# Kernel tuning notes

Measured on AMD Instinct MI355X. Metric: run time of the kernel, lower is better.

## Reference

```python
import jax, jax.numpy as jnp
import numpy as np

S, H, A = 8192, 4096, 1024

def setup_inputs() -> dict:
    key = jax.random.key(0)
    ks = jax.random.split(key, 8)
    return {
        "encoder_outputs": jax.random.normal(ks[0], (S, H), jnp.float32),
        "hidden": jax.random.normal(ks[1], (H,), jnp.float32),
        "U_w": jax.random.normal(ks[2], (A, H), jnp.float32) * (1.0 / np.sqrt(H)),
        "U_b": jax.random.normal(ks[3], (A,), jnp.float32) * 0.01,
        "W_w": jax.random.normal(ks[4], (A, H), jnp.float32) * (1.0 / np.sqrt(H)),
        "W_b": jax.random.normal(ks[5], (A,), jnp.float32) * 0.01,
        "V_w": jax.random.normal(ks[6], (1, A), jnp.float32) * (1.0 / np.sqrt(A)),
        "V_b": jax.random.normal(ks[7], (1,), jnp.float32) * 0.01,
    }

def reference(encoder_outputs, hidden, U_w, U_b, W_w, W_b, V_w, V_b):
    # Bahdanau additive attention ('add' mode).
    W_hidden = hidden @ W_w.T + W_b                      # [A]
    U_encode = encoder_outputs @ U_w.T + U_b             # [S, A]
    poly_tanh = jnp.tanh(U_encode + W_hidden)            # [S, A]
    scores = poly_tanh @ V_w.T + V_b                     # [S, 1]
    attn = jax.nn.softmax(scores, axis=0)                # softmax over sequence
    context = attn.T @ encoder_outputs                   # [1, H]
    return context[None]                                 # [1, 1, H] (matches torch bmm)
```

## Files before the change

kernel.cpp:

```cpp
#include <hip/hip_runtime.h>

typedef __attribute__((ext_vector_type(8))) short short8;
typedef __attribute__((ext_vector_type(4))) float f32x4;

#define S_DIM 8192
#define H_DIM 4096
#define A_DIM 1024

__device__ __forceinline__ short f2bf(float x) {
  unsigned u = __float_as_uint(x);
  u += 0x7fffu + ((u >> 16) & 1u);
  return (short)(u >> 16);
}

__device__ __forceinline__ float bf2f(short b) {
  return __uint_as_float(((unsigned)(unsigned short)b) << 16);
}

__device__ __forceinline__ void gload16(const void* g, void* l) {
  __builtin_amdgcn_global_load_lds(
      (const __attribute__((address_space(1))) void*)g,
      (__attribute__((address_space(3))) void*)l, 16, 0, 0);
}

__global__ __launch_bounds__(256) void comb_kernel(const float* __restrict__ hidden,
                                                   const float* __restrict__ Ww,
                                                   const float* __restrict__ Wb,
                                                   const float* __restrict__ Ub,
                                                   float* __restrict__ comb) {
  const int wave = threadIdx.x >> 6;
  const int lane = threadIdx.x & 63;
  const int a = blockIdx.x * 4 + wave;
  const float* row = Ww + (size_t)a * H_DIM;
  float acc = 0.f;
  for (int k = lane * 4; k < H_DIM; k += 64 * 4) {
    float4 w = *(const float4*)(row + k);
    float4 h = *(const float4*)(hidden + k);
    acc += w.x * h.x + w.y * h.y + w.z * h.z + w.w * h.w;
  }
  #pragma unroll
  for (int mk = 1; mk < 64; mk <<= 1) acc += __shfl_xor(acc, mk);
  if (lane == 0) comb[a] = acc + Wb[a] + Ub[a];
}

__global__ __launch_bounds__(256) void cvt_kernel(const float* __restrict__ src,
                                                  unsigned short* __restrict__ dst,
                                                  int n8) {
  const int stride = gridDim.x * blockDim.x;
  for (int i = blockIdx.x * blockDim.x + threadIdx.x; i < n8; i += stride) {
    float4 a = ((const float4*)src)[(size_t)i * 2];
    float4 b = ((const float4*)src)[(size_t)i * 2 + 1];
    short8 o;
    o[0] = f2bf(a.x); o[1] = f2bf(a.y); o[2] = f2bf(a.z); o[3] = f2bf(a.w);
    o[4] = f2bf(b.x); o[5] = f2bf(b.y); o[6] = f2bf(b.z); o[7] = f2bf(b.w);
    ((short8*)dst)[i] = o;
  }
}

__global__ __launch_bounds__(512, 2) void gemm_score_8p_kernel(
    const unsigned short* __restrict__ A,
    const unsigned short* __restrict__ B,
    const float* __restrict__ comb,
    const float* __restrict__ Vw,
    float* __restrict__ scores) {
  __shared__ __align__(16) unsigned short sA[3][256 * 64];
  __shared__ __align__(16) unsigned short sB[3][128 * 64];

  const int tid  = threadIdx.x;
  const int lane = tid & 63;
  const int wave = tid >> 6;
  const int wm = wave >> 1;
  const int wn = wave & 1;
  const int m0 = blockIdx.x * 256;
  const int n0 = blockIdx.y * 128;

  const int permEl = (((lane & 7) ^ (lane >> 3)) * 8);
  const unsigned short* gA = A + (size_t)(m0 + wave * 32 + (lane >> 3)) * H_DIM + permEl;
  const unsigned short* gB = B + (size_t)(n0 + wave * 16 + (lane >> 3)) * H_DIM + permEl;

  #define STAGE(kt, bf) do {                                                  \
    const unsigned short* pa_ = gA + (size_t)(kt) * 64;                       \
    const unsigned short* pb_ = gB + (size_t)(kt) * 64;                       \
    _Pragma("unroll")                                                         \
    for (int l_ = 0; l_ < 4; ++l_)                                            \
      gload16(pa_ + (size_t)l_ * 8 * H_DIM, &sA[bf][(wave * 4 + l_) * 512]);  \
    _Pragma("unroll")                                                         \
    for (int l_ = 0; l_ < 2; ++l_)                                            \
      gload16(pb_ + (size_t)l_ * 8 * H_DIM, &sB[bf][(wave * 2 + l_) * 512]);  \
  } while (0)

  const int rA  = lane & 15;
  const int grp = lane >> 4;
  const int lx  = lane & 7;

  f32x4 acc[4][4];
  const f32x4 zero = {0.f, 0.f, 0.f, 0.f};
  #pragma unroll
  for (int i = 0; i < 4; ++i)
    #pragma unroll
    for (int j = 0; j < 4; ++j) acc[i][j] = zero;

  STAGE(0, 0);
  STAGE(1, 1);
  asm volatile("s_waitcnt vmcnt(6)");
  __builtin_amdgcn_s_barrier();
  __builtin_amdgcn_sched_barrier(0);

  const int NT = H_DIM / 64;
  for (int t = 0; t < NT; ++t) {
    const int cur = t % 3;
    if (t + 2 < NT) STAGE(t + 2, (t + 2) % 3);

    const unsigned short* a_ = sA[cur];
    const unsigned short* b_ = sB[cur];
    #pragma unroll
    for (int ks = 0; ks < 2; ++ks) {
      short8 af[4], bfr[4];
      #pragma unroll
      for (int i = 0; i < 4; ++i)
        af[i] = *(const short8*)&a_[(wm * 64 + i * 16 + rA) * 64 + (((ks * 4 + grp) ^ lx) * 8)];
      #pragma unroll
      for (int j = 0; j < 4; ++j)
        bfr[j] = *(const short8*)&b_[(wn * 64 + j * 16 + rA) * 64 + (((ks * 4 + grp) ^ lx) * 8)];
      __builtin_amdgcn_s_setprio(1);
      #pragma unroll
      for (int i = 0; i < 4; ++i)
        #pragma unroll
        for (int j = 0; j < 4; ++j)
          acc[i][j] = __builtin_amdgcn_mfma_f32_16x16x32_bf16(af[i], bfr[j], acc[i][j], 0, 0, 0);
      __builtin_amdgcn_s_setprio(0);
    }

    __builtin_amdgcn_sched_barrier(0);
    if (t < NT - 2) asm volatile("s_waitcnt vmcnt(6)");
    else            asm volatile("s_waitcnt vmcnt(0)");
    __builtin_amdgcn_s_barrier();
    __builtin_amdgcn_sched_barrier(0);
  }
  #undef STAGE

  float vwv[4], cbv[4];
  #pragma unroll
  for (int j = 0; j < 4; ++j) {
    const int col = n0 + wn * 64 + j * 16 + rA;
    vwv[j] = Vw[col];
    cbv[j] = comb[col];
  }
  #pragma unroll
  for (int i = 0; i < 4; ++i) {
    #pragma unroll
    for (int r = 0; r < 4; ++r) {
      float s = 0.f;
      #pragma unroll
      for (int j = 0; j < 4; ++j)
        s += vwv[j] * tanhf(acc[i][j][r] + cbv[j]);
      s += __shfl_xor(s, 1);
      s += __shfl_xor(s, 2);
      s += __shfl_xor(s, 4);
      s += __shfl_xor(s, 8);
      if (rA == 0) {
        const int grow = m0 + wm * 64 + i * 16 + grp * 4 + r;
        atomicAdd(&scores[grow], s);
      }
    }
  }
}

__global__ __launch_bounds__(1024) void softmax_kernel(const float* __restrict__ scores,
                                                       float* __restrict__ attn) {
  __shared__ float redm[16];
  __shared__ float reds[16];
  const int tid = threadIdx.x;
  const int lane = tid & 63, wid = tid >> 6;
  float v[8];
  float m = -3.0e38f;
  #pragma unroll
  for (int i = 0; i < 8; ++i) { v[i] = scores[i * 1024 + tid]; m = fmaxf(m, v[i]); }
  #pragma unroll
  for (int mk = 1; mk < 64; mk <<= 1) m = fmaxf(m, __shfl_xor(m, mk));
  if (lane == 0) redm[wid] = m;
  __syncthreads();
  float M = redm[0];
  #pragma unroll
  for (int j = 1; j < 16; ++j) M = fmaxf(M, redm[j]);
  float e[8]; float s = 0.f;
  #pragma unroll
  for (int i = 0; i < 8; ++i) { e[i] = __expf(v[i] - M); s += e[i]; }
  #pragma unroll
  for (int mk = 1; mk < 64; mk <<= 1) s += __shfl_xor(s, mk);
  if (lane == 0) reds[wid] = s;
  __syncthreads();
  float T = 0.f;
  #pragma unroll
  for (int j = 0; j < 16; ++j) T += reds[j];
  const float inv = 1.f / T;
  #pragma unroll
  for (int i = 0; i < 8; ++i) attn[i * 1024 + tid] = e[i] * inv;
}

__global__ __launch_bounds__(256) void context_bf_kernel(const unsigned short* __restrict__ Ebf,
                                                         const float* __restrict__ attn,
                                                         float* __restrict__ partial) {
  const int h0 = (blockIdx.x * 256 + threadIdx.x) * 8;
  const int s0 = blockIdx.y * 64;
  float acc[8] = {0.f, 0.f, 0.f, 0.f, 0.f, 0.f, 0.f, 0.f};
  for (int s = s0; s < s0 + 64; ++s) {
    const float w = attn[s];
    short8 e = *(const short8*)(Ebf + (size_t)s * H_DIM + h0);
    #pragma unroll
    for (int j = 0; j < 8; ++j) acc[j] += w * bf2f(e[j]);
  }
  float* p = partial + (size_t)blockIdx.y * H_DIM + h0;
  #pragma unroll
  for (int j = 0; j < 8; ++j) p[j] = acc[j];
}

__global__ __launch_bounds__(256) void context_reduce_kernel(const float* __restrict__ partial,
                                                             float* __restrict__ out) {
  const int h = blockIdx.x * 256 + threadIdx.x;
  float acc = 0.f;
  #pragma unroll 8
  for (int y = 0; y < 128; ++y) acc += partial[(size_t)y * H_DIM + h];
  out[h] = acc;
}


#define LDSW 40
__global__ __launch_bounds__(256) void gemm_score_kernel(const float* __restrict__ E,
                                                         const float* __restrict__ Uw,
                                                         const float* __restrict__ comb,
                                                         const float* __restrict__ Vw,
                                                         float* __restrict__ scores) {
  __shared__ __align__(16) short sA[128 * LDSW];
  __shared__ __align__(16) short sB[128 * LDSW];
  const int tid  = threadIdx.x;
  const int lane = tid & 63;
  const int wave = tid >> 6;
  const int wm = wave >> 1, wn = wave & 1;
  const int m0 = blockIdx.x * 128;
  const int n0 = blockIdx.y * 128;
  const int sr = tid >> 1;
  const int sh = tid & 1;
  const float* gA = E  + (size_t)(m0 + sr) * H_DIM + sh * 16;
  const float* gB = Uw + (size_t)(n0 + sr) * H_DIM + sh * 16;
  alignas(16) float fa[16], fb[16];
  #pragma unroll
  for (int j = 0; j < 4; ++j) {
    *(float4*)&fa[j * 4] = *(const float4*)(gA + j * 4);
    *(float4*)&fb[j * 4] = *(const float4*)(gB + j * 4);
  }
  f32x4 acc[4][4];
  const f32x4 zero = {0.f, 0.f, 0.f, 0.f};
  #pragma unroll
  for (int i = 0; i < 4; ++i)
    #pragma unroll
    for (int j = 0; j < 4; ++j) acc[i][j] = zero;
  short* wA = &sA[sr * LDSW + sh * 16];
  short* wB = &sB[sr * LDSW + sh * 16];
  const int NK = H_DIM / 32;
  for (int kt = 0; kt < NK; ++kt) {
    short8 ca0, ca1, cb0, cb1;
    #pragma unroll
    for (int j = 0; j < 8; ++j) {
      ca0[j] = f2bf(fa[j]);     ca1[j] = f2bf(fa[8 + j]);
      cb0[j] = f2bf(fb[j]);     cb1[j] = f2bf(fb[8 + j]);
    }
    __syncthreads();
    *(short8*)(wA)     = ca0;
    *(short8*)(wA + 8) = ca1;
    *(short8*)(wB)     = cb0;
    *(short8*)(wB + 8) = cb1;
    __syncthreads();
    if (kt + 1 < NK) {
      const float* pA = gA + (kt + 1) * 32;
      const float* pB = gB + (kt + 1) * 32;
      #pragma unroll
      for (int j = 0; j < 4; ++j) {
        *(float4*)&fa[j * 4] = *(const float4*)(pA + j * 4);
        *(float4*)&fb[j * 4] = *(const float4*)(pB + j * 4);
      }
    }
    short8 af[4], bfr[4];
    #pragma unroll
    for (int i = 0; i < 4; ++i)
      af[i] = *(const short8*)&sA[(wm * 64 + i * 16 + (lane & 15)) * LDSW + (lane >> 4) * 8];
    #pragma unroll
    for (int j = 0; j < 4; ++j)
      bfr[j] = *(const short8*)&sB[(wn * 64 + j * 16 + (lane & 15)) * LDSW + (lane >> 4) * 8];
    #pragma unroll
    for (int i = 0; i < 4; ++i)
      #pragma unroll
      for (int j = 0; j < 4; ++j)
        acc[i][j] = __builtin_amdgcn_mfma_f32_16x16x32_bf16(af[i], bfr[j], acc[i][j], 0, 0, 0);
  }
  float vwv[4], cbv[4];
  #pragma unroll
  for (int j = 0; j < 4; ++j) {
    const int col = n0 + wn * 64 + j * 16 + (lane & 15);
    vwv[j] = Vw[col];
    cbv[j] = comb[col];
  }
  #pragma unroll
  for (int i = 0; i < 4; ++i) {
    #pragma unroll
    for (int r = 0; r < 4; ++r) {
      float s = 0.f;
      #pragma unroll
      for (int j = 0; j < 4; ++j)
        s += vwv[j] * tanhf(acc[i][j][r] + cbv[j]);
      s += __shfl_xor(s, 1);
      s += __shfl_xor(s, 2);
      s += __shfl_xor(s, 4);
      s += __shfl_xor(s, 8);
      if ((lane & 15) == 0) {
        const int grow = m0 + wm * 64 + i * 16 + (lane >> 4) * 4 + r;
        atomicAdd(&scores[grow], s);
      }
    }
  }
}

__global__ __launch_bounds__(256) void context_kernel(const float* __restrict__ E,
                                                      const float* __restrict__ attn,
                                                      float* __restrict__ out) {
  const int h  = blockIdx.x * 256 + threadIdx.x;
  const int s0 = blockIdx.y * 256;
  float acc = 0.f;
  #pragma unroll 4
  for (int s = s0; s < s0 + 256; ++s)
    acc += attn[s] * E[(size_t)s * H_DIM + h];
  atomicAdd(&out[h], acc);
}


extern "C" void kernel_launch(void* const* d_in, const int* in_sizes, int n_in,
                              void* d_out, int out_size, void* d_ws, size_t ws_size,
                              hipStream_t stream) {
  const float* E   = (const float*)d_in[0];
  const float* hid = (const float*)d_in[1];
  const float* Uw  = (const float*)d_in[2];
  const float* Ub  = (const float*)d_in[3];
  const float* Ww  = (const float*)d_in[4];
  const float* Wb  = (const float*)d_in[5];
  const float* Vw  = (const float*)d_in[6];

  float* out    = (float*)d_out;
  float* ws     = (float*)d_ws;
  float* comb   = ws;
  float* scores = ws + 1024;
  float* attn   = ws + 1024 + 8192;
  float* ctxp   = ws + 17408;
  const size_t CTXP = (size_t)128 * H_DIM;

  unsigned short* Ebf  = (unsigned short*)(ws + 17408 + CTXP);
  unsigned short* Uwbf = Ebf + (size_t)S_DIM * H_DIM;
  const size_t NEED = ((size_t)17408 + CTXP) * 4
                    + ((size_t)S_DIM + A_DIM) * H_DIM * 2;

  hipMemsetAsync(scores, 0, S_DIM * sizeof(float), stream);

  comb_kernel<<<A_DIM / 4, 256, 0, stream>>>(hid, Ww, Wb, Ub, comb);

  if (ws_size >= NEED) {
    cvt_kernel<<<2048, 256, 0, stream>>>(E, Ebf, (int)((size_t)S_DIM * H_DIM / 8));
    cvt_kernel<<<512, 256, 0, stream>>>(Uw, Uwbf, (int)((size_t)A_DIM * H_DIM / 8));

    gemm_score_8p_kernel<<<dim3(S_DIM / 256, A_DIM / 128), 512, 0, stream>>>(
        Ebf, Uwbf, comb, Vw, scores);

    softmax_kernel<<<1, 1024, 0, stream>>>(scores, attn);

    context_bf_kernel<<<dim3(H_DIM / 2048, S_DIM / 64), 256, 0, stream>>>(Ebf, attn, ctxp);
    context_reduce_kernel<<<H_DIM / 256, 256, 0, stream>>>(ctxp, out);
  } else {
    hipMemsetAsync(out, 0, (size_t)out_size * sizeof(float), stream);
    gemm_score_kernel<<<dim3(S_DIM / 128, A_DIM / 128), 256, 0, stream>>>(E, Uw, comb, Vw, scores);
    softmax_kernel<<<1, 1024, 0, stream>>>(scores, attn);
    context_kernel<<<dim3(H_DIM / 256, 32), 256, 0, stream>>>(E, attn, out);
  }
}
```

Baseline: 164.2 us.

## Split GEMM main loop into four barrier-synced phases interleaving loads and MFMAs

Restructures each K-tile iteration into four phases. Each phase issues a few LDS fragment reads and a slice of the next-tile global-to-LDS loads, then waits on barriers and runs 8 MFMAs, in the style of ping-pong scheduling across the two waves per SIMD. The global load mapping is also changed so each wave loads 8 consecutive rows per chunk instead of a 32-row strip. The goal is to spread memory issue between matrix ops and lower register pressure by holding only two A fragments at a time. The cost is more barriers per iteration (eight instead of one), which adds synchronisation overhead.

Result: slower. 171.9 us (+4.7%).

```diff
diff --git a/kernel.cpp b/kernel.cpp
--- a/kernel.cpp
+++ b/kernel.cpp
@@ -74,25 +74,46 @@
   const int m0 = blockIdx.x * 256;
   const int n0 = blockIdx.y * 128;
 
-  const int permEl = (((lane & 7) ^ (lane >> 3)) * 8);
-  const unsigned short* gA = A + (size_t)(m0 + wave * 32 + (lane >> 3)) * H_DIM + permEl;
-  const unsigned short* gB = B + (size_t)(n0 + wave * 16 + (lane >> 3)) * H_DIM + permEl;
-
-  #define STAGE(kt, bf) do {                                                  \
-    const unsigned short* pa_ = gA + (size_t)(kt) * 64;                       \
-    const unsigned short* pb_ = gB + (size_t)(kt) * 64;                       \
-    _Pragma("unroll")                                                         \
-    for (int l_ = 0; l_ < 4; ++l_)                                            \
-      gload16(pa_ + (size_t)l_ * 8 * H_DIM, &sA[bf][(wave * 4 + l_) * 512]);  \
-    _Pragma("unroll")                                                         \
-    for (int l_ = 0; l_ < 2; ++l_)                                            \
-      gload16(pb_ + (size_t)l_ * 8 * H_DIM, &sB[bf][(wave * 2 + l_) * 512]);  \
-  } while (0)
-
   const int rA  = lane & 15;
   const int grp = lane >> 4;
   const int lx  = lane & 7;
 
+  const int permEl = (((lane & 7) ^ (lane >> 3)) * 8);
+  const unsigned short* gA0 = A + (size_t)(m0 + wave * 8 + (lane >> 3)) * H_DIM + permEl;
+  const unsigned short* gB0 = B + (size_t)(n0 + wave * 8 + (lane >> 3)) * H_DIM + permEl;
+
+  #define STAGE_A(kt, bf, c) \
+    gload16(gA0 + (size_t)(c) * 64 * H_DIM + (size_t)(kt) * 64, \
+            &sA[bf][((c) * 64 + wave * 8) * 64])
+  #define STAGE_B(kt, bf, c) \
+    gload16(gB0 + (size_t)(c) * 64 * H_DIM + (size_t)(kt) * 64, \
+            &sB[bf][((c) * 64 + wave * 8) * 64])
+  #define STAGE_TILE(kt, bf) do { \
+    STAGE_A(kt, bf, 0); STAGE_A(kt, bf, 1); STAGE_A(kt, bf, 2); STAGE_A(kt, bf, 3); \
+    STAGE_B(kt, bf, 0); STAGE_B(kt, bf, 1); } while (0)
+
+  #define DSREAD_B(ks) do { _Pragma("unroll") \
+    for (int j = 0; j < 4; ++j) \
+      bfr[j] = *(const short8*)&b_[(wn * 64 + j * 16 + rA) * 64 + ((((ks) * 4 + grp) ^ lx) * 8)]; \
+    } while (0)
+  #define DSREAD_A(ks, i0) do { \
+    af0 = *(const short8*)&a_[(wm * 64 + (i0) * 16 + rA) * 64 + ((((ks) * 4 + grp) ^ lx) * 8)]; \
+    af1 = *(const short8*)&a_[(wm * 64 + ((i0) + 1) * 16 + rA) * 64 + ((((ks) * 4 + grp) ^ lx) * 8)]; \
+    } while (0)
+  #define MFMA8(i0) do { \
+    __builtin_amdgcn_s_setprio(1); \
+    _Pragma("unroll") \
+    for (int j = 0; j < 4; ++j) { \
+      acc[(i0)][j]     = __builtin_amdgcn_mfma_f32_16x16x32_bf16(af0, bfr[j], acc[(i0)][j], 0, 0, 0); \
+      acc[(i0) + 1][j] = __builtin_amdgcn_mfma_f32_16x16x32_bf16(af1, bfr[j], acc[(i0) + 1][j], 0, 0, 0); \
+    } \
+    __builtin_amdgcn_s_setprio(0); } while (0)
+  #define PH_PRE()  do { __builtin_amdgcn_s_barrier(); \
+    asm volatile("s_waitcnt lgkmcnt(0)" ::: "memory"); \
+    __builtin_amdgcn_sched_barrier(0); } while (0)
+  #define PH_POST() do { __builtin_amdgcn_s_barrier(); \
+    __builtin_amdgcn_sched_barrier(0); } while (0)
+
   f32x4 acc[4][4];
   const f32x4 zero = {0.f, 0.f, 0.f, 0.f};
   #pragma unroll
@@ -100,8 +121,8 @@
     #pragma unroll
     for (int j = 0; j < 4; ++j) acc[i][j] = zero;
 
-  STAGE(0, 0);
-  STAGE(1, 1);
+  STAGE_TILE(0, 0);
+  STAGE_TILE(1, 1);
   asm volatile("s_waitcnt vmcnt(6)");
   __builtin_amdgcn_s_barrier();
   __builtin_amdgcn_sched_barrier(0);
@@ -109,35 +130,45 @@
   const int NT = H_DIM / 64;
   for (int t = 0; t < NT; ++t) {
     const int cur = t % 3;
-    if (t + 2 < NT) STAGE(t + 2, (t + 2) % 3);
-
+    const int pf  = (t + 2) % 3;
+    const bool stg = (t + 2 < NT);
     const unsigned short* a_ = sA[cur];
     const unsigned short* b_ = sB[cur];
-    #pragma unroll
-    for (int ks = 0; ks < 2; ++ks) {
-      short8 af[4], bfr[4];
-      #pragma unroll
-      for (int i = 0; i < 4; ++i)
-        af[i] = *(const short8*)&a_[(wm * 64 + i * 16 + rA) * 64 + (((ks * 4 + grp) ^ lx) * 8)];
-      #pragma unroll
-      for (int j = 0; j < 4; ++j)
-        bfr[j] = *(const short8*)&b_[(wn * 64 + j * 16 + rA) * 64 + (((ks * 4 + grp) ^ lx) * 8)];
-      __builtin_amdgcn_s_setprio(1);
-      #pragma unroll
-      for (int i = 0; i < 4; ++i)
-        #pragma unroll
-        for (int j = 0; j < 4; ++j)
-          acc[i][j] = __builtin_amdgcn_mfma_f32_16x16x32_bf16(af[i], bfr[j], acc[i][j], 0, 0, 0);
-      __builtin_amdgcn_s_setprio(0);
-    }
-
-    __builtin_amdgcn_sched_barrier(0);
-    if (t < NT - 2) asm volatile("s_waitcnt vmcnt(6)");
-    else            asm volatile("s_waitcnt vmcnt(0)");
-    __builtin_amdgcn_s_barrier();
-    __builtin_amdgcn_sched_barrier(0);
-  }
-  #undef STAGE
+    short8 af0, af1, bfr[4];
+
+    DSREAD_B(0); DSREAD_A(0, 0);
+    if (stg) { STAGE_A(t + 2, pf, 0); STAGE_A(t + 2, pf, 1); }
+    PH_PRE();
+    MFMA8(0);
+    PH_POST();
+
+    DSREAD_A(0, 2);
+    if (stg) { STAGE_A(t + 2, pf, 2); STAGE_A(t + 2, pf, 3); }
+    PH_PRE();
+    MFMA8(2);
+    PH_POST();
+
+    DSREAD_B(1); DSREAD_A(1, 0);
+    if (stg) { STAGE_B(t + 2, pf, 0); STAGE_B(t + 2, pf, 1); }
+    PH_PRE();
+    MFMA8(0);
+    PH_POST();
+
+    DSREAD_A(1, 2);
+    PH_PRE();
+    MFMA8(2);
+    if (t + 2 < NT)      asm volatile("s_waitcnt vmcnt(6)");
+    else if (t + 1 < NT) asm volatile("s_waitcnt vmcnt(0)");
+    PH_POST();
+  }
+  #undef STAGE_A
+  #undef STAGE_B
+  #undef STAGE_TILE
+  #undef DSREAD_A
+  #undef DSREAD_B
+  #undef MFMA8
+  #undef PH_PRE
+  #undef PH_POST
 
   float vwv[4], cbv[4];
   #pragma unroll
```
